# Performance work log

Hardware: AMD Instinct MI355X
Metric: run time of the kernel (lower is better)

The kernel has to match this reference:

```python
import jax, jax.numpy as jnp
import numpy as np

K = 9                      # num_keypoints
NC = 1
NA = 1
NB, NH, NW = 64, 32, 32
NUM_LABELS = 2 * K + 3     # 21
NOOBJ, OBJ = 1.0, 5.0      # noobject_scale, object_scale
SIL = 0.6                  # sil_thresh
TH, SHARP, IMW, IMH = 80.0, 2.0, 640.0, 480.0
EPS = 1e-5


def setup_inputs() -> dict:
    key = jax.random.key(0)
    output = jax.random.normal(key, (NB, NA * (2 * K + 1 + NC), NH, NW), jnp.float32)
    # Build targets: 8 valid objects per image, keypoint-0 on distinct grid cells.
    rng = np.random.default_rng(0)
    nT = 8
    tgt = np.zeros((NB, 50, NUM_LABELS), np.float32)
    cells = np.stack([rng.permutation(NH * NW)[:nT] for _ in range(NB)])  # unique cells
    gi = cells % NW
    gj = cells // NW
    x0 = (gi + rng.uniform(0.05, 0.95, (NB, nT))) / NW
    y0 = (gj + rng.uniform(0.05, 0.95, (NB, nT))) / NH
    tgt[:, :nT, 1] = x0
    tgt[:, :nT, 2] = y0
    for i in range(1, K):
        tgt[:, :nT, 2 * i + 1] = np.clip(x0 + rng.uniform(-0.08, 0.08, (NB, nT)), 1e-3, 0.999)
        tgt[:, :nT, 2 * i + 2] = np.clip(y0 + rng.uniform(-0.08, 0.08, (NB, nT)), 1e-3, 0.999)
    target = jnp.asarray(tgt.reshape(NB, 50 * NUM_LABELS))
    return {"output": output, "target": target, "epoch": 20}


def _corner_conf(diff):
    # diff: [..., 2K] differences of normalized corner coords -> mean keypoint confidence
    d = diff.reshape(diff.shape[:-1] + (K, 2)) * jnp.array([IMW, IMH], diff.dtype)
    dist = jnp.sqrt(jnp.sum(d * d, axis=-1))  # [..., K] pixel distance
    conf = (jnp.exp(SHARP * (1.0 - dist / TH)) - 1.0) / (jnp.exp(SHARP) - 1.0 + EPS)
    return jnp.mean(jnp.where(dist < TH, conf, 0.0), axis=-1)


def _region_loss(output, target, epoch):
    out = output.reshape(NB, NA, 2 * K + 1 + NC, NH, NW)[:, 0]  # nA == 1
    xs = out[:, 0:2 * K:2]   # [nB, K, nH, nW]
    ys = out[:, 1:2 * K:2]
    xs = jnp.concatenate([jax.nn.sigmoid(xs[:, :1]), xs[:, 1:]], axis=1)  # only kp0 sigmoided
    ys = jnp.concatenate([jax.nn.sigmoid(ys[:, :1]), ys[:, 1:]], axis=1)
    conf = jax.nn.sigmoid(out[:, 2 * K])  # [nB, nH, nW]

    gx = jnp.arange(NW, dtype=output.dtype)
    gy = jnp.arange(NH, dtype=output.dtype)
    px = (xs + gx[None, None, None, :]) / NW
    py = (ys + gy[None, None, :, None]) / NH
    # interleave x0,y0,x1,y1,... -> [nB, nH*nW, 2K]
    pc = jnp.stack([px, py], axis=2).transpose(0, 3, 4, 1, 2).reshape(NB, NH * NW, 2 * K)
    pc_sg = jax.lax.stop_gradient(pc)  # build_targets uses .data (detached)

    tgt = target.reshape(NB, 50, NUM_LABELS)
    # serial break at first zero x-coord -> cumulative validity
    valid = jnp.cumprod((tgt[:, :, 1] != 0).astype(jnp.float32), axis=1) > 0  # [nB,50]
    gt = tgt[:, :, 1:1 + 2 * K]  # [nB, 50, 2K]

    # --- silence-threshold pass: max corner confidence over targets per anchor ---
    diff = gt[:, :, None, :] - pc_sg[:, None, :, :]      # [nB,50,nH*nW,2K]
    confs = _corner_conf(diff)                            # [nB,50,nH*nW]
    cur = jnp.max(jnp.where(valid[:, :, None], confs, 0.0), axis=1)  # [nB,nH*nW]
    conf_mask = jnp.where(cur > SIL, 0.0, NOOBJ).reshape(NB, NH, NW)

    # --- target assignment at keypoint-0 cell (best_n == 0) ---
    gxk = gt[:, :, 0::2] * NW   # [nB,50,K]
    gyk = gt[:, :, 1::2] * NH
    gi0 = jnp.floor(gxk[:, :, 0]).astype(jnp.int32)
    gj0 = jnp.floor(gyk[:, :, 0]).astype(jnp.int32)
    gi0 = jnp.where(valid, gi0, NW)   # out-of-bounds -> dropped by scatter
    gj0 = jnp.where(valid, gj0, NH)
    b_idx = jnp.broadcast_to(jnp.arange(NB)[:, None], (NB, 50))

    coord_mask = jnp.zeros((NB, NH, NW), output.dtype).at[b_idx, gj0, gi0].set(1.0)
    conf_mask = conf_mask.at[b_idx, gj0, gi0].set(OBJ)
    tx = jnp.zeros((NB, NH, NW, K), output.dtype).at[b_idx, gj0, gi0].set(
        gxk - gi0[:, :, None].astype(output.dtype))
    ty = jnp.zeros((NB, NH, NW, K), output.dtype).at[b_idx, gj0, gi0].set(
        gyk - gj0[:, :, None].astype(output.dtype))

    flat = jnp.clip(gj0 * NW + gi0, 0, NH * NW - 1)       # [nB,50]
    pb = jnp.take_along_axis(pc_sg, flat[:, :, None], axis=1)  # [nB,50,2K]
    conf_gt = _corner_conf(gt - pb)                        # [nB,50]
    tconf = jnp.zeros((NB, NH, NW), output.dtype).at[b_idx, gj0, gi0].set(conf_gt)

    # --- losses (coord_scale = 1) ---
    xs_t = xs.transpose(0, 2, 3, 1)  # [nB,nH,nW,K]
    ys_t = ys.transpose(0, 2, 3, 1)
    cm = coord_mask[..., None]
    loss_x = 0.5 * jnp.sum(((xs_t - tx) * cm) ** 2)
    loss_y = 0.5 * jnp.sum(((ys_t - ty) * cm) ** 2)
    loss_conf = 0.5 * jnp.sum(((conf - tconf) * jnp.sqrt(conf_mask)) ** 2)
    if epoch > 15:  # pretrain_num_epochs; epoch is a static Python int
        return loss_x + loss_y + loss_conf
    return loss_x + loss_y


def reference(output, target, epoch):
    return _region_loss(output, target, epoch)
```

## Files before the change

### kernel.cpp

```cpp
#include <hip/hip_runtime.h>
#include <math.h>

#define K     9
#define NB    64
#define NH    32
#define NW    32
#define NCELLS (NH * NW)
#define NT    50
#define NUM_LABELS (2 * K + 3)
#define CH    (2 * K + 2)
#define THF   80.0f
#define SHARPF 2.0f
#define SILF  0.6f
#define NOOBJF 1.0f
#define OBJF  5.0f
#define IMWF  640.0f
#define IMHF  480.0f

__global__ __launch_bounds__(256) void region_loss_kernel(
    const float* __restrict__ outp,
    const float* __restrict__ tgt,
    const int*   __restrict__ epoch_p,
    float*       __restrict__ loss_out)
{
    __shared__ float sX[NT][K];
    __shared__ float sY[NT][K];
    __shared__ float sTx[NT][K];
    __shared__ float sTy[NT][K];
    __shared__ int   sGi[NT], sGj[NT], sFlag[NT];
    __shared__ int   sNv;
    __shared__ float sRed[4];

    const int b    = blockIdx.x >> 2;
    const int tid  = threadIdx.x;
    const int cell = ((blockIdx.x & 3) << 8) + tid;
    const int gi   = cell & (NW - 1);
    const int gj   = cell >> 5;

    if (tid < NT) {
        const float* tp = tgt + (size_t)b * NT * NUM_LABELS + tid * NUM_LABELS + 1;
        float x0 = tp[0];
        sFlag[tid] = (x0 != 0.0f) ? 1 : 0;
        int gi0 = (int)floorf(tp[0] * (float)NW);
        int gj0 = (int)floorf(tp[1] * (float)NH);
        sGi[tid] = gi0;
        sGj[tid] = gj0;
        #pragma unroll
        for (int k = 0; k < K; k++) {
            float xk = tp[2 * k];
            float yk = tp[2 * k + 1];
            sX[tid][k]  = xk * IMWF;
            sY[tid][k]  = yk * IMHF;
            sTx[tid][k] = xk * (float)NW - (float)gi0;
            sTy[tid][k] = yk * (float)NH - (float)gj0;
        }
    }
    __syncthreads();
    if (tid == 0) {
        int nv = 0;
        while (nv < NT && sFlag[nv]) nv++;
        sNv = nv;
    }
    __syncthreads();
    const int nv = sNv;

    const float* ob = outp + ((size_t)b * CH) * NCELLS + cell;
    float xs[K], ys[K];
    #pragma unroll
    for (int k = 0; k < K; k++) {
        xs[k] = ob[(2 * k) * NCELLS];
        ys[k] = ob[(2 * k + 1) * NCELLS];
    }
    float conf_logit = ob[(2 * K) * NCELLS];

    xs[0] = 1.0f / (1.0f + __expf(-xs[0]));
    ys[0] = 1.0f / (1.0f + __expf(-ys[0]));
    const float conf = 1.0f / (1.0f + __expf(-conf_logit));

    float PX[K], PY[K];
    #pragma unroll
    for (int k = 0; k < K; k++) {
        PX[k] = (xs[k] + (float)gi) * (IMWF / (float)NW);
        PY[k] = (ys[k] + (float)gj) * (IMHF / (float)NH);
    }

    const float inv_den = 1.0f / (__expf(SHARPF) - 1.0f + 1e-5f);
    float cur    = 0.0f;
    float tconf  = 0.0f;
    int   tmatch = -1;

    for (int t = 0; t < nv; t++) {
        float s = 0.0f;
        #pragma unroll
        for (int k = 0; k < K; k++) {
            float dx = sX[t][k] - PX[k];
            float dy = sY[t][k] - PY[k];
            float d2 = dx * dx + dy * dy;
            if (d2 < THF * THF) {
                float dist = sqrtf(d2);
                s += (__expf(SHARPF * (1.0f - dist * (1.0f / THF))) - 1.0f) * inv_den;
            }
        }
        float ct = s * (1.0f / (float)K);
        cur = fmaxf(cur, ct);
        if (gi == sGi[t] && gj == sGj[t]) {
            tconf  = ct;
            tmatch = t;
        }
    }

    float mask = (tmatch >= 0) ? OBJF : ((cur > SILF) ? 0.0f : NOOBJF);

    const int epoch = *epoch_p;
    float d = conf - tconf;
    float local = (epoch > 15) ? (0.5f * d * d * mask) : 0.0f;

    if (tmatch >= 0) {
        float sxy = 0.0f;
        #pragma unroll
        for (int k = 0; k < K; k++) {
            float ex = xs[k] - sTx[tmatch][k];
            float ey = ys[k] - sTy[tmatch][k];
            sxy += ex * ex + ey * ey;
        }
        local += 0.5f * sxy;
    }

    #pragma unroll
    for (int off = 32; off > 0; off >>= 1)
        local += __shfl_down(local, off, 64);
    const int wave = tid >> 6;
    const int lane = tid & 63;
    if (lane == 0) sRed[wave] = local;
    __syncthreads();
    if (tid == 0) {
        float s = sRed[0] + sRed[1] + sRed[2] + sRed[3];
        atomicAdd(loss_out, s);
    }
}

extern "C" void kernel_launch(void* const* d_in, const int* in_sizes, int n_in,
                              void* d_out, int out_size, void* d_ws, size_t ws_size,
                              hipStream_t stream) {
    const float* outp  = (const float*)d_in[0];
    const float* tgt   = (const float*)d_in[1];
    const int*   epoch = (const int*)d_in[2];
    float* loss = (float*)d_out;

    hipMemsetAsync(loss, 0, sizeof(float) * (size_t)out_size, stream);
    region_loss_kernel<<<dim3(NB * 4), dim3(256), 0, stream>>>(outp, tgt, epoch, loss);
}
```

Baseline: 69.14 us.

## Use one 1024-thread block per image and parallelize target staging

Each block now covers a whole image (1024 cells) rather than a quarter, so the per-image target staging runs once instead of four times. Target parsing is spread across 450 threads (one per target/keypoint pair) instead of 50 threads each looping over keypoints. The global output loads are issued before the shared-memory staging so they overlap it, and the final reduction uses a 16-lane shuffle. The trade-off is only 64 blocks on a GPU with many CUs, which lowers parallelism and occupancy, and 1024-thread blocks limit registers per thread.

```diff
diff --git a/kernel.cpp b/kernel.cpp
--- a/kernel.cpp
+++ b/kernel.cpp
@@ -17,7 +17,7 @@
 #define IMWF  640.0f
 #define IMHF  480.0f
 
-__global__ __launch_bounds__(256) void region_loss_kernel(
+__global__ __launch_bounds__(1024) void region_loss_kernel(
     const float* __restrict__ outp,
     const float* __restrict__ tgt,
     const int*   __restrict__ epoch_p,
@@ -29,30 +29,40 @@
     __shared__ float sTy[NT][K];
     __shared__ int   sGi[NT], sGj[NT], sFlag[NT];
     __shared__ int   sNv;
-    __shared__ float sRed[4];
+    __shared__ float sRed[16];
 
-    const int b    = blockIdx.x >> 2;
+    const int b    = blockIdx.x;
     const int tid  = threadIdx.x;
-    const int cell = ((blockIdx.x & 3) << 8) + tid;
+    const int cell = tid;
     const int gi   = cell & (NW - 1);
     const int gj   = cell >> 5;
 
-    if (tid < NT) {
-        const float* tp = tgt + (size_t)b * NT * NUM_LABELS + tid * NUM_LABELS + 1;
-        float x0 = tp[0];
-        sFlag[tid] = (x0 != 0.0f) ? 1 : 0;
+    const float* ob = outp + ((size_t)b * CH) * NCELLS + cell;
+    float xs[K], ys[K];
+    #pragma unroll
+    for (int k = 0; k < K; k++) {
+        xs[k] = ob[(2 * k) * NCELLS];
+        ys[k] = ob[(2 * k + 1) * NCELLS];
+    }
+    float conf_logit = ob[(2 * K) * NCELLS];
+
+    const float* tb = tgt + (size_t)b * NT * NUM_LABELS;
+    if (tid < NT * K) {
+        const int t = tid / K;
+        const int k = tid - t * K;
+        const float* tp = tb + t * NUM_LABELS + 1;
+        float xk = tp[2 * k];
+        float yk = tp[2 * k + 1];
         int gi0 = (int)floorf(tp[0] * (float)NW);
         int gj0 = (int)floorf(tp[1] * (float)NH);
-        sGi[tid] = gi0;
-        sGj[tid] = gj0;
-        #pragma unroll
-        for (int k = 0; k < K; k++) {
-            float xk = tp[2 * k];
-            float yk = tp[2 * k + 1];
-            sX[tid][k]  = xk * IMWF;
-            sY[tid][k]  = yk * IMHF;
-            sTx[tid][k] = xk * (float)NW - (float)gi0;
-            sTy[tid][k] = yk * (float)NH - (float)gj0;
+        sX[t][k]  = xk * IMWF;
+        sY[t][k]  = yk * IMHF;
+        sTx[t][k] = xk * (float)NW - (float)gi0;
+        sTy[t][k] = yk * (float)NH - (float)gj0;
+        if (k == 0) {
+            sGi[t] = gi0;
+            sGj[t] = gj0;
+            sFlag[t] = (tp[0] != 0.0f) ? 1 : 0;
         }
     }
     __syncthreads();
@@ -63,15 +73,6 @@
     }
     __syncthreads();
     const int nv = sNv;
-
-    const float* ob = outp + ((size_t)b * CH) * NCELLS + cell;
-    float xs[K], ys[K];
-    #pragma unroll
-    for (int k = 0; k < K; k++) {
-        xs[k] = ob[(2 * k) * NCELLS];
-        ys[k] = ob[(2 * k + 1) * NCELLS];
-    }
-    float conf_logit = ob[(2 * K) * NCELLS];
 
     xs[0] = 1.0f / (1.0f + __expf(-xs[0]));
     ys[0] = 1.0f / (1.0f + __expf(-ys[0]));
@@ -133,9 +134,12 @@
     const int lane = tid & 63;
     if (lane == 0) sRed[wave] = local;
     __syncthreads();
-    if (tid == 0) {
-        float s = sRed[0] + sRed[1] + sRed[2] + sRed[3];
-        atomicAdd(loss_out, s);
+    if (wave == 0) {
+        float s = (lane < 16) ? sRed[lane] : 0.0f;
+        #pragma unroll
+        for (int off = 8; off > 0; off >>= 1)
+            s += __shfl_down(s, off, 64);
+        if (lane == 0) atomicAdd(loss_out, s);
     }
 }
 
@@ -148,5 +152,5 @@
     float* loss = (float*)d_out;
 
     hipMemsetAsync(loss, 0, sizeof(float) * (size_t)out_size, stream);
-    region_loss_kernel<<<dim3(NB * 4), dim3(256), 0, stream>>>(outp, tgt, epoch, loss);
+    region_loss_kernel<<<dim3(NB), dim3(1024), 0, stream>>>(outp, tgt, epoch, loss);
 }
```

Measured after the change: 71.78 us. +3.8%, slower.
